# Performance work log

Measured on AMD Instinct MI355X. Metric: run time of the kernel, lower is better.

The kernel has to match this reference:

```python
import jax, jax.numpy as jnp
import numpy as np

# config derived from init_kwargs: batch_sizes=[2048,2048], rs=[32,128], num_adapters=[32,32]
B1, B2, MULT = 2048, 2048, 4            # group1 tokens (r_mult=1), group2 tokens (r_mult=128/32=4)
IN_F, OUT_F, R_MIN = 4096, 4096, 32
NA1, NA2 = 32, 32
N_SPLIT_ADAPTERS = NA1 + NA2 * MULT      # 160 rank-min slices
LORA_BATCH = B1 + B2 * MULT              # 10240 gathered rows


def setup_inputs() -> dict:
    key = jax.random.key(0)
    k1, k2, k3, k4, k5 = jax.random.split(key, 5)
    x = jax.random.normal(k1, (B1 + B2, 1, IN_F), dtype=jnp.float16)
    lora_A = (jax.random.normal(k2, (N_SPLIT_ADAPTERS, IN_F, R_MIN), dtype=jnp.float16) * jnp.float16(0.02))
    lora_B = (jax.random.normal(k3, (N_SPLIT_ADAPTERS, R_MIN, OUT_F), dtype=jnp.float16) * jnp.float16(0.02))
    # group1: one row per token; group2: each token repeated MULT times (rank split)
    xids = jnp.concatenate([
        jnp.arange(B1, dtype=jnp.int32),
        jnp.repeat(jnp.arange(B1, B1 + B2, dtype=jnp.int32), MULT),
    ])
    # group1 adapters occupy slice ids [0, NA1); group2 adapter j occupies NA1 + j*MULT .. +MULT-1
    w1 = jax.random.randint(k4, (B1,), 0, NA1, dtype=jnp.int32)
    j = jax.random.randint(k5, (B2,), 0, NA2, dtype=jnp.int32)
    w2 = ((jnp.int32(NA1) + j * MULT)[:, None] + jnp.arange(MULT, dtype=jnp.int32)[None, :]).reshape(-1)
    wids = jnp.concatenate([w1, w2])
    return {"x": x, "xids": xids, "wids": wids, "lora_A": lora_A, "lora_B": lora_B}


def reference(x, xids, wids, lora_A, lora_B):
    xg = jnp.take(x, xids, axis=0)          # (L, 1, IN_F)
    A = jnp.take(lora_A, wids, axis=0)      # (L, IN_F, R_MIN)
    Bw = jnp.take(lora_B, wids, axis=0)     # (L, R_MIN, OUT_F)
    y = jnp.einsum('lpi,lir->lpr', xg, A)   # (L, 1, R_MIN)
    y = jnp.einsum('lpr,lro->lpo', y, Bw) * 2.0  # (L, 1, OUT_F), scaling factor 2.0
    # split + sum combine: group1 passes through, group2 sums each block of MULT rank-slices
    z1 = y[:B1]                                          # (B1, 1, OUT_F)
    z2 = y[B1:].reshape(B2, MULT, 1, OUT_F).sum(axis=1)  # (B2, 1, OUT_F)
    return jnp.concatenate([z1, z2], axis=0)             # (B1+B2, 1, OUT_F)
```

## Files before the change

kernel.cpp:

```cpp
#include <hip/hip_runtime.h>

#define IN_F   4096
#define OUT_F  4096
#define RK     32
#define NB1    2048
#define LBATCH 10240
#define MAXB   2048
#define TILES  4

typedef __attribute__((ext_vector_type(2))) __fp16 h2;
typedef __attribute__((ext_vector_type(8))) __fp16 h8;
typedef __attribute__((ext_vector_type(4))) float  f4;


__global__ __launch_bounds__(256) void bin_rows(const int* __restrict__ wids,
                                                int* cnt1, int* cnt2,
                                                int* list1, int* list2) {
    int t = blockIdx.x * 256 + threadIdx.x;
    if (t < NB1) {
        int w = wids[t];
        int p = atomicAdd(&cnt1[w], 1);
        list1[w * MAXB + p] = t;
    } else {
        int i = t - NB1;
        int j = (wids[NB1 + 4 * i] - 32) >> 2;
        int p = atomicAdd(&cnt2[j], 1);
        list2[j * MAXB + p] = i;
    }
}

template<bool P2>
__device__ __forceinline__ void s1_body(const float* __restrict__ x,
                                        const float* __restrict__ A,
                                        float* __restrict__ r,
                                        __fp16 (*At)[128][40],
                                        const int* rowid,
                                        int g, int k0, int tz, int n) {
    constexpr int NT = P2 ? 8 : 2;
    constexpr int KL = P2 ? 16 : 4;

    int t    = threadIdx.x;
    int lane = t & 63;
    int w    = t >> 6;
    int m    = lane & 15;
    int kg   = lane >> 4;

    int xr = rowid[16 * w + m];
    const float* xb = x + (size_t)(P2 ? NB1 + xr : xr) * IN_F + k0 + kg * 8;

    int C  = t & (P2 ? 127 : 31);
    int kh = t >> (P2 ? 7 : 5);
    const float* asrc;
    if constexpr (P2)
        asrc = A + ((size_t)(32 + 4 * g + (C >> 5)) * IN_F + k0 + kh * KL) * RK + (C & 31);
    else
        asrc = A + ((size_t)g * IN_F + k0 + kh * KL) * RK + C;

    f4 acc[NT];
    #pragma unroll
    for (int ct = 0; ct < NT; ++ct) acc[ct] = (f4){0.f, 0.f, 0.f, 0.f};

    f4 xf0 = *(const f4*)xb;
    f4 xf1 = *(const f4*)(xb + 4);
    {
        float v[KL];
        #pragma unroll
        for (int q = 0; q < KL; ++q) v[q] = asrc[q * RK];
        #pragma unroll
        for (int q = 0; q < KL / 2; ++q)
            *(h2*)&At[0][C][kh * KL + 2 * q] = __builtin_amdgcn_cvt_pkrtz(v[2 * q], v[2 * q + 1]);
    }
    __syncthreads();

    #pragma unroll
    for (int s = 0; s < 8; ++s) {
        float vn[KL];
        f4 nx0, nx1;
        if (s < 7) {
            const float* as2 = asrc + (size_t)(s + 1) * 32 * RK;
            #pragma unroll
            for (int q = 0; q < KL; ++q) vn[q] = as2[q * RK];
            nx0 = *(const f4*)(xb + (s + 1) * 32);
            nx1 = *(const f4*)(xb + (s + 1) * 32 + 4);
        }
        h8 xa;
        {
            union { h8 v8; h2 h[4]; } u;
            u.h[0] = __builtin_amdgcn_cvt_pkrtz(xf0.x, xf0.y);
            u.h[1] = __builtin_amdgcn_cvt_pkrtz(xf0.z, xf0.w);
            u.h[2] = __builtin_amdgcn_cvt_pkrtz(xf1.x, xf1.y);
            u.h[3] = __builtin_amdgcn_cvt_pkrtz(xf1.z, xf1.w);
            xa = u.v8;
        }
        int b = s & 1;
        #pragma unroll
        for (int ct = 0; ct < NT; ++ct) {
            h8 bf = *(const h8*)&At[b][ct * 16 + m][kg * 8];
            acc[ct] = __builtin_amdgcn_mfma_f32_16x16x32_f16(xa, bf, acc[ct], 0, 0, 0);
        }
        if (s < 7) {
            #pragma unroll
            for (int q = 0; q < KL / 2; ++q)
                *(h2*)&At[b ^ 1][C][kh * KL + 2 * q] = __builtin_amdgcn_cvt_pkrtz(vn[2 * q], vn[2 * q + 1]);
            xf0 = nx0; xf1 = nx1;
        }
        __syncthreads();
    }

    #pragma unroll
    for (int q = 0; q < 4; ++q) {
        int br = 16 * w + 4 * kg + q;
        int it = 64 * tz + br;
        if (it < n) {
            int rid = rowid[br];
            #pragma unroll
            for (int ct = 0; ct < NT; ++ct) {
                int c = ct * 16 + m;
                size_t off = P2 ? ((size_t)(NB1 + 4 * rid + (c >> 5)) * RK + (c & 31))
                                : ((size_t)rid * RK + c);
                atomicAdd(&r[off], acc[ct][q]);
            }
        }
    }
}

__global__ __launch_bounds__(256, 3) void s1_all(const float* __restrict__ x,
                                                 const float* __restrict__ A,
                                                 const int*   __restrict__ cnt,
                                                 const int*   __restrict__ list,
                                                 float*       __restrict__ r) {
    __shared__ __align__(16) __fp16 At[2][128][40];
    __shared__ int rowid[64];
    int g  = blockIdx.x;
    int tz = blockIdx.z;
    int n  = cnt[g];
    if (64 * tz >= n) return;
    if (threadIdx.x < 64) {
        int it = 64 * tz + threadIdx.x;
        rowid[threadIdx.x] = list[g * MAXB + (it < n ? it : n - 1)];
    }
    __syncthreads();
    int k0 = blockIdx.y * 256;
    if (g < 32) s1_body<false>(x, A, r, At, rowid, g, k0, tz, n);
    else        s1_body<true >(x, A, r, At, rowid, g - 32, k0, tz, n);
}

template<bool P2>
__device__ __forceinline__ void s2_body(const float* __restrict__ r,
                                        const float* __restrict__ B,
                                        float* __restrict__ out,
                                        __fp16 (*Bt)[128][40],
                                        const int* rowid,
                                        int g, int ot, int tz, int n) {
    constexpr int NS = P2 ? 4 : 1;

    int t    = threadIdx.x;
    int lane = t & 63;
    int w    = t >> 6;
    int m    = lane & 15;
    int kg   = lane >> 4;

    int rid0 = rowid[16 * w + m];

    f4 ra[NS], rb[NS];
    #pragma unroll
    for (int kc = 0; kc < NS; ++kc) {
        const float* rp = r + (P2 ? (size_t)(NB1 + 4 * rid0 + kc) * RK
                                  : (size_t)rid0 * RK) + kg * 8;
        ra[kc] = *(const f4*)rp;
        rb[kc] = *(const f4*)(rp + 4);
    }

    int oc = t & 127;
    int kh = t >> 7;
    float v[16];
    {
        int a = P2 ? (32 + 4 * g) : g;
        const float* s0 = B + ((size_t)a * RK + kh * 16) * OUT_F + ot * 128 + oc;
        #pragma unroll
        for (int q = 0; q < 16; ++q) v[q] = s0[q * OUT_F];
    }

    h8 rf[NS];
    #pragma unroll
    for (int kc = 0; kc < NS; ++kc) {
        h8 f;
        f[0] = (__fp16)ra[kc].x; f[1] = (__fp16)ra[kc].y;
        f[2] = (__fp16)ra[kc].z; f[3] = (__fp16)ra[kc].w;
        f[4] = (__fp16)rb[kc].x; f[5] = (__fp16)rb[kc].y;
        f[6] = (__fp16)rb[kc].z; f[7] = (__fp16)rb[kc].w;
        rf[kc] = f;
    }

    #pragma unroll
    for (int q = 0; q < 8; ++q)
        *(h2*)&Bt[0][oc][kh * 16 + 2 * q] = __builtin_amdgcn_cvt_pkrtz(v[2 * q], v[2 * q + 1]);
    __syncthreads();

    f4 acc[8];
    #pragma unroll
    for (int ct = 0; ct < 8; ++ct) acc[ct] = (f4){0.f, 0.f, 0.f, 0.f};

    #pragma unroll
    for (int kc = 0; kc < NS; ++kc) {
        float vn[16];
        if (kc < NS - 1) {
            int a = 32 + 4 * g + kc + 1;
            const float* sn = B + ((size_t)a * RK + kh * 16) * OUT_F + ot * 128 + oc;
            #pragma unroll
            for (int q = 0; q < 16; ++q) vn[q] = sn[q * OUT_F];
        }
        int b = kc & 1;
        #pragma unroll
        for (int ct = 0; ct < 8; ++ct) {
            h8 bf = *(const h8*)&Bt[b][ct * 16 + m][kg * 8];
            acc[ct] = __builtin_amdgcn_mfma_f32_16x16x32_f16(rf[kc], bf, acc[ct], 0, 0, 0);
        }
        if (kc < NS - 1) {
            #pragma unroll
            for (int q = 0; q < 8; ++q)
                *(h2*)&Bt[b ^ 1][oc][kh * 16 + 2 * q] = __builtin_amdgcn_cvt_pkrtz(vn[2 * q], vn[2 * q + 1]);
        }
        __syncthreads();
    }

    #pragma unroll
    for (int q = 0; q < 4; ++q) {
        int br = 16 * w + 4 * kg + q;
        int it = 64 * tz + br;
        if (it < n) {
            int orow = P2 ? (NB1 + rowid[br]) : rowid[br];
            float* op = out + (size_t)orow * OUT_F + ot * 128 + m;
            #pragma unroll
            for (int ct = 0; ct < 8; ++ct)
                op[ct * 16] = 2.f * acc[ct][q];
        }
    }
}

__global__ __launch_bounds__(256, 3) void s2_all(const float* __restrict__ r,
                                                 const float* __restrict__ B,
                                                 const int*   __restrict__ cnt,
                                                 const int*   __restrict__ list,
                                                 float*       __restrict__ out) {
    __shared__ __align__(16) __fp16 Bt[2][128][40];
    __shared__ int rowid[64];
    int g  = blockIdx.x;
    int ot = blockIdx.y;
    int tz = blockIdx.z;
    int n  = cnt[g];
    if (64 * tz >= n) return;
    if (threadIdx.x < 64) {
        int it = 64 * tz + threadIdx.x;
        rowid[threadIdx.x] = list[g * MAXB + (it < n ? it : n - 1)];
    }
    __syncthreads();
    if (g < 32) s2_body<false>(r, B, out, Bt, rowid, g, ot, tz, n);
    else        s2_body<true >(r, B, out, Bt, rowid, g - 32, ot, tz, n);
}

extern "C" void kernel_launch(void* const* d_in, const int* in_sizes, int n_in,
                              void* d_out, int out_size, void* d_ws, size_t ws_size,
                              hipStream_t stream) {
    const float* x    = (const float*)d_in[0];
    const int*   wids = (const int*)  d_in[2];
    const float* A    = (const float*)d_in[3];
    const float* Bm   = (const float*)d_in[4];
    float* out = (float*)d_out;

    int* wsI   = (int*)d_ws;
    int* cnt1  = wsI;
    int* cnt2  = wsI + 32;
    int* list1 = wsI + 64;
    int* list2 = list1 + 32 * MAXB;
    float* r   = (float*)(list2 + 32 * MAXB);

    hipMemsetAsync(cnt1, 0, 64 * sizeof(int), stream);
    hipMemsetAsync(r, 0, (size_t)LBATCH * RK * sizeof(float), stream);

    bin_rows<<<dim3(16), dim3(256), 0, stream>>>(wids, cnt1, cnt2, list1, list2);
    s1_all<<<dim3(64, 16, TILES), dim3(256), 0, stream>>>(x, A, cnt1, list1, r);
    s2_all<<<dim3(64, 32, TILES), dim3(256), 0, stream>>>(r, Bm, cnt1, list1, out);
}
```

Before: 296.6 us.

## Replace split-K atomics with per-split slabs, coalesce A loads, loop output tiles

Binning now happens in one block with shared-memory counters, which removes both memsets. Stage 1 uses fewer K splits (up to 8 instead of 16, sized to fit the workspace). Each split writes plain stores into its own slab instead of doing global atomicAdd, and stage 2 sums the slabs when it loads its input. A tiles are now loaded as f4 vectors into an XOR-swizzled LDS layout to cut bank conflicts. Each stage-2 block covers 4 output tiles so the rank vector is loaded once and reused, at the cost of a single LDS buffer with extra syncs and a serial slab reduction.

```diff
diff --git a/kernel.cpp b/kernel.cpp
--- a/kernel.cpp
+++ b/kernel.cpp
@@ -7,81 +7,91 @@
 #define LBATCH 10240
 #define MAXB   2048
 #define TILES  4
+#define LRK    (LBATCH * RK)
 
 typedef __attribute__((ext_vector_type(2))) __fp16 h2;
 typedef __attribute__((ext_vector_type(8))) __fp16 h8;
 typedef __attribute__((ext_vector_type(4))) float  f4;
 
 
-__global__ __launch_bounds__(256) void bin_rows(const int* __restrict__ wids,
-                                                int* cnt1, int* cnt2,
-                                                int* list1, int* list2) {
-    int t = blockIdx.x * 256 + threadIdx.x;
-    if (t < NB1) {
-        int w = wids[t];
-        int p = atomicAdd(&cnt1[w], 1);
-        list1[w * MAXB + p] = t;
-    } else {
-        int i = t - NB1;
-        int j = (wids[NB1 + 4 * i] - 32) >> 2;
-        int p = atomicAdd(&cnt2[j], 1);
-        list2[j * MAXB + p] = i;
-    }
+__global__ __launch_bounds__(1024) void bin_rows(const int* __restrict__ wids,
+                                                 int* __restrict__ cnt,
+                                                 int* __restrict__ list) {
+    __shared__ int lc[64];
+    int t = threadIdx.x;
+    if (t < 64) lc[t] = 0;
+    __syncthreads();
+    for (int it = t; it < 4096; it += 1024) {
+        int b, v;
+        if (it < NB1) { b = wids[it]; v = it; }
+        else { int i = it - NB1; b = 32 + ((wids[NB1 + 4 * i] - 32) >> 2); v = i; }
+        int p = atomicAdd(&lc[b], 1);
+        list[b * MAXB + p] = v;
+    }
+    __syncthreads();
+    if (t < 64) cnt[t] = lc[t];
 }
 
 template<bool P2>
 __device__ __forceinline__ void s1_body(const float* __restrict__ x,
                                         const float* __restrict__ A,
-                                        float* __restrict__ r,
+                                        float* __restrict__ slab,
                                         __fp16 (*At)[128][40],
                                         const int* rowid,
-                                        int g, int k0, int tz, int n) {
-    constexpr int NT = P2 ? 8 : 2;
-    constexpr int KL = P2 ? 16 : 4;
-
-    int t    = threadIdx.x;
-    int lane = t & 63;
-    int w    = t >> 6;
-    int m    = lane & 15;
-    int kg   = lane >> 4;
+                                        int g, int k0, int nsteps, int tz, int n) {
+    constexpr int NT  = P2 ? 8 : 2;
+    constexpr int NTK = P2 ? 2 : 1;
+
+    int t = threadIdx.x, lane = t & 63, w = t >> 6, m = lane & 15, kg = lane >> 4;
 
     int xr = rowid[16 * w + m];
     const float* xb = x + (size_t)(P2 ? NB1 + xr : xr) * IN_F + k0 + kg * 8;
 
-    int C  = t & (P2 ? 127 : 31);
-    int kh = t >> (P2 ? 7 : 5);
-    const float* asrc;
-    if constexpr (P2)
-        asrc = A + ((size_t)(32 + 4 * g + (C >> 5)) * IN_F + k0 + kh * KL) * RK + (C & 31);
-    else
-        asrc = A + ((size_t)g * IN_F + k0 + kh * KL) * RK + C;
+    int tkp[NTK], tc0[NTK];
+    const float* ap[NTK];
+    #pragma unroll
+    for (int p = 0; p < NTK; ++p) {
+        int tau = P2 ? (t + 256 * p) : (t & 127);
+        int kp  = P2 ? (tau >> 5) : (tau >> 3);
+        int c4  = P2 ? (tau & 31) : (tau & 7);
+        int c0  = 4 * c4;
+        tkp[p] = kp; tc0[p] = c0;
+        int ad  = P2 ? (32 + 4 * g + (c0 >> 5)) : g;
+        ap[p] = A + ((size_t)ad * IN_F + k0 + 2 * kp) * RK + (c0 & 31);
+    }
 
     f4 acc[NT];
     #pragma unroll
     for (int ct = 0; ct < NT; ++ct) acc[ct] = (f4){0.f, 0.f, 0.f, 0.f};
 
-    f4 xf0 = *(const f4*)xb;
-    f4 xf1 = *(const f4*)(xb + 4);
-    {
-        float v[KL];
-        #pragma unroll
-        for (int q = 0; q < KL; ++q) v[q] = asrc[q * RK];
-        #pragma unroll
-        for (int q = 0; q < KL / 2; ++q)
-            *(h2*)&At[0][C][kh * KL + 2 * q] = __builtin_amdgcn_cvt_pkrtz(v[2 * q], v[2 * q + 1]);
-    }
-    __syncthreads();
-
-    #pragma unroll
-    for (int s = 0; s < 8; ++s) {
-        float vn[KL];
-        f4 nx0, nx1;
-        if (s < 7) {
-            const float* as2 = asrc + (size_t)(s + 1) * 32 * RK;
-            #pragma unroll
-            for (int q = 0; q < KL; ++q) vn[q] = as2[q * RK];
-            nx0 = *(const f4*)(xb + (s + 1) * 32);
-            nx1 = *(const f4*)(xb + (s + 1) * 32 + 4);
+    f4 xf0 = *(const f4*)xb, xf1 = *(const f4*)(xb + 4);
+    f4 a0[NTK], a1[NTK];
+    #pragma unroll
+    for (int p = 0; p < NTK; ++p) { a0[p] = *(const f4*)ap[p]; a1[p] = *(const f4*)(ap[p] + RK); }
+    #pragma unroll
+    for (int p = 0; p < NTK; ++p) {
+        int k = 2 * tkp[p];
+        #pragma unroll
+        for (int j = 0; j < 4; ++j) {
+            int c  = tc0[p] + j;
+            int kb = (k >> 3) ^ ((c >> 3) & 3);
+            *(h2*)&At[0][c][kb * 8 + (k & 7)] = __builtin_amdgcn_cvt_pkrtz(a0[p][j], a1[p][j]);
+        }
+    }
+    __syncthreads();
+
+    for (int s = 0; s < nsteps; ++s) {
+        int  b    = s & 1;
+        bool more = (s + 1 < nsteps);
+        f4 nx0, nx1, n0[NTK], n1[NTK];
+        if (more) {
+            nx0 = *(const f4*)(xb + (size_t)(s + 1) * 32);
+            nx1 = *(const f4*)(xb + (size_t)(s + 1) * 32 + 4);
+            #pragma unroll
+            for (int p = 0; p < NTK; ++p) {
+                const float* q = ap[p] + (size_t)(s + 1) * 32 * RK;
+                n0[p] = *(const f4*)q; n1[p] = *(const f4*)(q + RK);
+            }
         }
         h8 xa;
         {
@@ -92,16 +102,24 @@
             u.h[3] = __builtin_amdgcn_cvt_pkrtz(xf1.z, xf1.w);
             xa = u.v8;
         }
-        int b = s & 1;
         #pragma unroll
         for (int ct = 0; ct < NT; ++ct) {
-            h8 bf = *(const h8*)&At[b][ct * 16 + m][kg * 8];
+            int c  = ct * 16 + m;
+            int kb = kg ^ ((c >> 3) & 3);
+            h8 bf  = *(const h8*)&At[b][c][kb * 8];
             acc[ct] = __builtin_amdgcn_mfma_f32_16x16x32_f16(xa, bf, acc[ct], 0, 0, 0);
         }
-        if (s < 7) {
-            #pragma unroll
-            for (int q = 0; q < KL / 2; ++q)
-                *(h2*)&At[b ^ 1][C][kh * KL + 2 * q] = __builtin_amdgcn_cvt_pkrtz(vn[2 * q], vn[2 * q + 1]);
+        if (more) {
+            #pragma unroll
+            for (int p = 0; p < NTK; ++p) {
+                int k = 2 * tkp[p];
+                #pragma unroll
+                for (int j = 0; j < 4; ++j) {
+                    int c  = tc0[p] + j;
+                    int kb = (k >> 3) ^ ((c >> 3) & 3);
+                    *(h2*)&At[b ^ 1][c][kb * 8 + (k & 7)] = __builtin_amdgcn_cvt_pkrtz(n0[p][j], n1[p][j]);
+                }
+            }
             xf0 = nx0; xf1 = nx1;
         }
         __syncthreads();
@@ -118,17 +136,18 @@
                 int c = ct * 16 + m;
                 size_t off = P2 ? ((size_t)(NB1 + 4 * rid + (c >> 5)) * RK + (c & 31))
                                 : ((size_t)rid * RK + c);
-                atomicAdd(&r[off], acc[ct][q]);
-            }
-        }
-    }
-}
-
-__global__ __launch_bounds__(256, 3) void s1_all(const float* __restrict__ x,
+                slab[off] = acc[ct][q];
+            }
+        }
+    }
+}
+
+__global__ __launch_bounds__(256, 4) void s1_all(const float* __restrict__ x,
                                                  const float* __restrict__ A,
                                                  const int*   __restrict__ cnt,
                                                  const int*   __restrict__ list,
-                                                 float*       __restrict__ r) {
+                                                 float*       __restrict__ slabs,
+                                                 int nsteps) {
     __shared__ __align__(16) __fp16 At[2][128][40];
     __shared__ int rowid[64];
     int g  = blockIdx.x;
@@ -140,123 +159,118 @@
         rowid[threadIdx.x] = list[g * MAXB + (it < n ? it : n - 1)];
     }
     __syncthreads();
-    int k0 = blockIdx.y * 256;
-    if (g < 32) s1_body<false>(x, A, r, At, rowid, g, k0, tz, n);
-    else        s1_body<true >(x, A, r, At, rowid, g - 32, k0, tz, n);
+    int k0 = blockIdx.y * nsteps * 32;
+    float* slab = slabs + (size_t)blockIdx.y * LRK;
+    if (g < 32) s1_body<false>(x, A, slab, At, rowid, g, k0, nsteps, tz, n);
+    else        s1_body<true >(x, A, slab, At, rowid, g - 32, k0, nsteps, tz, n);
 }
 
 template<bool P2>
-__device__ __forceinline__ void s2_body(const float* __restrict__ r,
+__device__ __forceinline__ void s2_body(const float* __restrict__ slabs, int nslab,
                                         const float* __restrict__ B,
                                         float* __restrict__ out,
-                                        __fp16 (*Bt)[128][40],
+                                        __fp16 (*Bt)[40],
                                         const int* rowid,
-                                        int g, int ot, int tz, int n) {
-    constexpr int NS = P2 ? 4 : 1;
-
-    int t    = threadIdx.x;
-    int lane = t & 63;
-    int w    = t >> 6;
-    int m    = lane & 15;
-    int kg   = lane >> 4;
-
+                                        int g, int ot0, int tz, int n) {
+    constexpr int NS  = P2 ? 4 : 1;
+    constexpr int NPH = P2 ? 16 : 4;
+
+    int t = threadIdx.x, lane = t & 63, w = t >> 6, m = lane & 15, kg = lane >> 4;
     int rid0 = rowid[16 * w + m];
 
-    f4 ra[NS], rb[NS];
+    h8 rf[NS];
     #pragma unroll
     for (int kc = 0; kc < NS; ++kc) {
-        const float* rp = r + (P2 ? (size_t)(NB1 + 4 * rid0 + kc) * RK
-                                  : (size_t)rid0 * RK) + kg * 8;
-        ra[kc] = *(const f4*)rp;
-        rb[kc] = *(const f4*)(rp + 4);
-    }
-
-    int oc = t & 127;
-    int kh = t >> 7;
-    float v[16];
+        size_t ro = P2 ? (size_t)(NB1 + 4 * rid0 + kc) : (size_t)rid0;
+        const float* rp = slabs + ro * RK + kg * 8;
+        f4 sa = *(const f4*)rp, sb = *(const f4*)(rp + 4);
+        for (int s = 1; s < nslab; ++s) {
+            const float* q2 = rp + (size_t)s * LRK;
+            sa += *(const f4*)q2; sb += *(const f4*)(q2 + 4);
+        }
+        h8 f;
+        f[0] = (__fp16)sa.x; f[1] = (__fp16)sa.y; f[2] = (__fp16)sa.z; f[3] = (__fp16)sa.w;
+        f[4] = (__fp16)sb.x; f[5] = (__fp16)sb.y; f[6] = (__fp16)sb.z; f[7] = (__fp16)sb.w;
+        rf[kc] = f;
+    }
+
+    int oc = t & 127, kh = t >> 7;
+
+    float v[16], vn[16];
     {
         int a = P2 ? (32 + 4 * g) : g;
-        const float* s0 = B + ((size_t)a * RK + kh * 16) * OUT_F + ot * 128 + oc;
+        const float* s0 = B + ((size_t)a * RK + kh * 16) * OUT_F + (size_t)ot0 * 128 + oc;
         #pragma unroll
         for (int q = 0; q < 16; ++q) v[q] = s0[q * OUT_F];
     }
 
-    h8 rf[NS];
-    #pragma unroll
-    for (int kc = 0; kc < NS; ++kc) {
-        h8 f;
-        f[0] = (__fp16)ra[kc].x; f[1] = (__fp16)ra[kc].y;
-        f[2] = (__fp16)ra[kc].z; f[3] = (__fp16)ra[kc].w;
-        f[4] = (__fp16)rb[kc].x; f[5] = (__fp16)rb[kc].y;
-        f[6] = (__fp16)rb[kc].z; f[7] = (__fp16)rb[kc].w;
-        rf[kc] = f;
-    }
-
-    #pragma unroll
-    for (int q = 0; q < 8; ++q)
-        *(h2*)&Bt[0][oc][kh * 16 + 2 * q] = __builtin_amdgcn_cvt_pkrtz(v[2 * q], v[2 * q + 1]);
-    __syncthreads();
-
     f4 acc[8];
     #pragma unroll
     for (int ct = 0; ct < 8; ++ct) acc[ct] = (f4){0.f, 0.f, 0.f, 0.f};
 
     #pragma unroll
-    for (int kc = 0; kc < NS; ++kc) {
-        float vn[16];
-        if (kc < NS - 1) {
-            int a = 32 + 4 * g + kc + 1;
-            const float* sn = B + ((size_t)a * RK + kh * 16) * OUT_F + ot * 128 + oc;
+    for (int ph = 0; ph < NPH; ++ph) {
+        int oti = P2 ? (ph >> 2) : ph;
+        int kc  = P2 ? (ph & 3) : 0;
+        __syncthreads();
+        #pragma unroll
+        for (int q = 0; q < 8; ++q)
+            *(h2*)&Bt[oc][kh * 16 + 2 * q] = __builtin_amdgcn_cvt_pkrtz(v[2 * q], v[2 * q + 1]);
+        if (ph + 1 < NPH) {
+            int noti = P2 ? ((ph + 1) >> 2) : (ph + 1);
+            int nkc  = P2 ? ((ph + 1) & 3) : 0;
+            int a = P2 ? (32 + 4 * g + nkc) : g;
+            const float* sn = B + ((size_t)a * RK + kh * 16) * OUT_F + (size_t)(ot0 + noti) * 128 + oc;
             #pragma unroll
             for (int q = 0; q < 16; ++q) vn[q] = sn[q * OUT_F];
         }
-        int b = kc & 1;
+        __syncthreads();
         #pragma unroll
         for (int ct = 0; ct < 8; ++ct) {
-            h8 bf = *(const h8*)&Bt[b][ct * 16 + m][kg * 8];
+            h8 bf = *(const h8*)&Bt[ct * 16 + m][kg * 8];
             acc[ct] = __builtin_amdgcn_mfma_f32_16x16x32_f16(rf[kc], bf, acc[ct], 0, 0, 0);
         }
-        if (kc < NS - 1) {
-            #pragma unroll
-            for (int q = 0; q < 8; ++q)
-                *(h2*)&Bt[b ^ 1][oc][kh * 16 + 2 * q] = __builtin_amdgcn_cvt_pkrtz(vn[2 * q], vn[2 * q + 1]);
-        }
-        __syncthreads();
-    }
-
-    #pragma unroll
-    for (int q = 0; q < 4; ++q) {
-        int br = 16 * w + 4 * kg + q;
-        int it = 64 * tz + br;
-        if (it < n) {
-            int orow = P2 ? (NB1 + rowid[br]) : rowid[br];
-            float* op = out + (size_t)orow * OUT_F + ot * 128 + m;
-            #pragma unroll
-            for (int ct = 0; ct < 8; ++ct)
-                op[ct * 16] = 2.f * acc[ct][q];
-        }
-    }
-}
-
-__global__ __launch_bounds__(256, 3) void s2_all(const float* __restrict__ r,
+        if (kc == NS - 1) {
+            #pragma unroll
+            for (int q = 0; q < 4; ++q) {
+                int br = 16 * w + 4 * kg + q;
+                int it = 64 * tz + br;
+                if (it < n) {
+                    int orow = P2 ? (NB1 + rowid[br]) : rowid[br];
+                    float* op = out + (size_t)orow * OUT_F + (size_t)(ot0 + oti) * 128 + m;
+                    #pragma unroll
+                    for (int ct = 0; ct < 8; ++ct)
+                        op[ct * 16] = 2.f * acc[ct][q];
+                }
+            }
+            #pragma unroll
+            for (int ct = 0; ct < 8; ++ct) acc[ct] = (f4){0.f, 0.f, 0.f, 0.f};
+        }
+        #pragma unroll
+        for (int q = 0; q < 16; ++q) v[q] = vn[q];
+    }
+}
+
+__global__ __launch_bounds__(256, 3) void s2_all(const float* __restrict__ slabs,
+                                                 int nslab,
                                                  const float* __restrict__ B,
                                                  const int*   __restrict__ cnt,
                                                  const int*   __restrict__ list,
                                                  float*       __restrict__ out) {
-    __shared__ __align__(16) __fp16 Bt[2][128][40];
+    __shared__ __align__(16) __fp16 Bt[128][40];
     __shared__ int rowid[64];
-    int g  = blockIdx.x;
-    int ot = blockIdx.y;
-    int tz = blockIdx.z;
-    int n  = cnt[g];
+    int g   = blockIdx.x;
+    int ot0 = blockIdx.y * 4;
+    int tz  = blockIdx.z;
+    int n   = cnt[g];
     if (64 * tz >= n) return;
     if (threadIdx.x < 64) {
         int it = 64 * tz + threadIdx.x;
         rowid[threadIdx.x] = list[g * MAXB + (it < n ? it : n - 1)];
     }
     __syncthreads();
-    if (g < 32) s2_body<false>(r, B, out, Bt, rowid, g, ot, tz, n);
-    else        s2_body<true >(r, B, out, Bt, rowid, g - 32, ot, tz, n);
+    if (g < 32) s2_body<false>(slabs, nslab, B, out, Bt, rowid, g, ot0, tz, n);
+    else        s2_body<true >(slabs, nslab, B, out, Bt, rowid, g - 32, ot0, tz, n);
 }
 
 extern "C" void kernel_launch(void* const* d_in, const int* in_sizes, int n_in,
@@ -268,17 +282,17 @@
     const float* Bm   = (const float*)d_in[4];
     float* out = (float*)d_out;
 
-    int* wsI   = (int*)d_ws;
-    int* cnt1  = wsI;
-    int* cnt2  = wsI + 32;
-    int* list1 = wsI + 64;
-    int* list2 = list1 + 32 * MAXB;
-    float* r   = (float*)(list2 + 32 * MAXB);
-
-    hipMemsetAsync(cnt1, 0, 64 * sizeof(int), stream);
-    hipMemsetAsync(r, 0, (size_t)LBATCH * RK * sizeof(float), stream);
-
-    bin_rows<<<dim3(16), dim3(256), 0, stream>>>(wids, cnt1, cnt2, list1, list2);
-    s1_all<<<dim3(64, 16, TILES), dim3(256), 0, stream>>>(x, A, cnt1, list1, r);
-    s2_all<<<dim3(64, 32, TILES), dim3(256), 0, stream>>>(r, Bm, cnt1, list1, out);
-}
+    int* wsI  = (int*)d_ws;
+    int* cnt  = wsI;
+    int* list = wsI + 64;
+    float* slabs = (float*)(list + 64 * MAXB);
+
+    size_t fixed = (size_t)(64 + 64 * MAXB) * sizeof(int);
+    int ks = 8;
+    while (ks > 1 && fixed + (size_t)ks * LRK * sizeof(float) > ws_size) ks >>= 1;
+    int nsteps = 128 / ks;
+
+    bin_rows<<<dim3(1), dim3(1024), 0, stream>>>(wids, cnt, list);
+    s1_all<<<dim3(64, ks, TILES), dim3(256), 0, stream>>>(x, A, cnt, list, slabs, nsteps);
+    s2_all<<<dim3(64, 8, TILES), dim3(256), 0, stream>>>(slabs, ks, Bm, cnt, list, out);
+}
```

Result: no change. 292.8 us (-1.3%).
